# Performance work log

Hardware: AMD Instinct MI355X
Metric: run time of the kernel (lower is better)

The kernel has to match this reference:

```python
import jax, jax.numpy as jnp
import numpy as np

N = 50000      # nodes
E = 800000     # edges (avg degree 16)
D = 256        # d_model
H = 8          # heads
C = D // H     # per-head channels = 32
DE = 64        # edge feature dim
NEG_SLOPE = 0.2
EPS = 1e-5


def setup_inputs() -> dict:
    key = jax.random.key(0)
    ks = jax.random.split(key, 12)
    s = 0.05
    return {
        "x": jax.random.normal(ks[0], (N, D), jnp.float32),
        "edge_attr": jax.random.normal(ks[1], (E, DE), jnp.float32),
        "edge_index": jax.random.randint(ks[2], (2, E), 0, N, dtype=jnp.int32),
        # GATv2Conv params (torch Linear layout: [out, in])
        "W_l": jax.random.normal(ks[3], (H * C, D), jnp.float32) * s,   # lin_l (source)
        "b_l": jnp.zeros((H * C,), jnp.float32),
        "W_r": jax.random.normal(ks[4], (H * C, D), jnp.float32) * s,   # lin_r (target)
        "b_r": jnp.zeros((H * C,), jnp.float32),
        "W_e": jax.random.normal(ks[5], (H * C, DE), jnp.float32) * s,  # lin_edge (no bias)
        "att": jax.random.normal(ks[6], (H, C), jnp.float32) * s,       # attention vector a
        "W_res": jax.random.normal(ks[7], (H * C, D), jnp.float32) * s, # residual Linear (no bias)
        "bias": jnp.zeros((H * C,), jnp.float32),                        # conv output bias
        "gamma": jnp.ones((D,), jnp.float32),                            # LayerNorm weight
        "beta": jnp.zeros((D,), jnp.float32),                            # LayerNorm bias
    }


def reference(x, edge_attr, W_l, b_l, W_r, b_r, W_e, att, W_res, bias, gamma, beta, edge_index):
    src = edge_index[0]  # j (messages flow source -> target)
    dst = edge_index[1]  # i

    xl = (x @ W_l.T + b_l).reshape(N, H, C)   # source transform
    xr = (x @ W_r.T + b_r).reshape(N, H, C)   # target transform
    ee = (edge_attr @ W_e.T).reshape(E, H, C)  # edge embedding

    # GATv2 attention logits per edge/head
    g = jax.nn.leaky_relu(xl[src] + xr[dst] + ee, NEG_SLOPE)  # [E, H, C]
    alpha = jnp.einsum("ehc,hc->eh", g, att)                   # [E, H]

    # segment softmax over incoming edges of each target node
    amax = jax.ops.segment_max(alpha, dst, num_segments=N)     # [N, H] (-inf for empty)
    ealpha = jnp.exp(alpha - amax[dst])
    denom = jax.ops.segment_sum(ealpha, dst, num_segments=N)   # [N, H]
    alpha = ealpha / jnp.where(denom > 0, denom, 1.0)[dst]

    # weighted message aggregation (scatter-add)
    msg = xl[src] * alpha[:, :, None]                          # [E, H, C]
    out = jax.ops.segment_sum(msg, dst, num_segments=N)        # [N, H, C]

    out = out.reshape(N, H * C) + x @ W_res.T + bias           # concat heads + residual + bias

    # LayerNorm over last dim
    mu = out.mean(-1, keepdims=True)
    var = ((out - mu) ** 2).mean(-1, keepdims=True)
    return (out - mu) * jax.lax.rsqrt(var + EPS) * gamma + beta
```

## Files before the change

### kernel.cpp

```cpp
#include <hip/hip_runtime.h>

#define N_NODES 50000
#define N_EDGES 800000
#define D_MODEL 256
#define H_HEADS 8
#define C_CH 32
#define DE_DIM 64
#define NEG_SLOPE 0.2f
#define LN_EPS 1e-5f
#define TILES (N_EDGES / 64)
#define AGG_K 32

typedef float  f32x4  __attribute__((ext_vector_type(4)));
typedef short  bf16x8 __attribute__((ext_vector_type(8)));

static __device__ __forceinline__ unsigned short f2bf(float f) {
    unsigned int u = __float_as_uint(f);
    u += 0x7fffu + ((u >> 16) & 1u);
    return (unsigned short)(u >> 16);
}
static __device__ __forceinline__ float bf2f(unsigned short s) {
    return __uint_as_float(((unsigned int)s) << 16);
}
static __device__ __forceinline__ bf16x8 load_cvt8(const float* __restrict__ p) {
    float4 a = *(const float4*)p;
    float4 b = *(const float4*)(p + 4);
    bf16x8 r;
    r[0] = (short)f2bf(a.x); r[1] = (short)f2bf(a.y);
    r[2] = (short)f2bf(a.z); r[3] = (short)f2bf(a.w);
    r[4] = (short)f2bf(b.x); r[5] = (short)f2bf(b.y);
    r[6] = (short)f2bf(b.z); r[7] = (short)f2bf(b.w);
    return r;
}

__global__ __launch_bounds__(256) void cvt_bf16_kernel(const float* __restrict__ in,
                                                       unsigned short* __restrict__ out,
                                                       int n8) {
    int g = blockIdx.x * 256 + threadIdx.x;
    if (g < n8) {
        bf16x8 v = load_cvt8(in + (size_t)g * 8);
        *(bf16x8*)(out + (size_t)g * 8) = v;
    }
}

__global__ __launch_bounds__(256) void node_gemm(const unsigned short* __restrict__ xbf,
                                                 const unsigned short* __restrict__ Wbf,
                                                 const float* __restrict__ bl,
                                                 const float* __restrict__ br,
                                                 unsigned short* __restrict__ xl,
                                                 unsigned short* __restrict__ xr,
                                                 float* __restrict__ res) {
    int tid = threadIdx.x;
    int lane = tid & 63, wv = tid >> 6;
    int quad = lane >> 4, l15 = lane & 15;
    int rowTile = blockIdx.x * 64;
    int which = blockIdx.y;
    const unsigned short* W = Wbf + (size_t)which * 65536;
    int colBase = wv * 64;

    f32x4 acc[4][4];
#pragma unroll
    for (int r = 0; r < 4; r++)
#pragma unroll
        for (int c = 0; c < 4; c++) acc[r][c] = (f32x4){0.f, 0.f, 0.f, 0.f};

#pragma unroll 1
    for (int k8 = 0; k8 < 8; ++k8) {
        int kb = k8 * 32 + quad * 8;
        bf16x8 af[4], bfr[4];
#pragma unroll
        for (int r = 0; r < 4; r++) {
            int row = rowTile + r * 16 + l15;
            if (row > N_NODES - 1) row = N_NODES - 1;
            af[r] = *(const bf16x8*)(xbf + (size_t)row * D_MODEL + kb);
        }
#pragma unroll
        for (int c = 0; c < 4; c++) {
            int col = colBase + c * 16 + l15;
            bfr[c] = *(const bf16x8*)(W + (size_t)col * D_MODEL + kb);
        }
#pragma unroll
        for (int r = 0; r < 4; r++)
#pragma unroll
            for (int c = 0; c < 4; c++)
                acc[r][c] = __builtin_amdgcn_mfma_f32_16x16x32_bf16(af[r], bfr[c], acc[r][c], 0, 0, 0);
    }

    float bv[4];
#pragma unroll
    for (int c = 0; c < 4; c++) {
        int col = colBase + c * 16 + l15;
        bv[c] = (which == 0) ? bl[col] : (which == 1 ? br[col] : 0.f);
    }
#pragma unroll
    for (int r = 0; r < 4; r++) {
#pragma unroll
        for (int g = 0; g < 4; g++) {
            int row = rowTile + r * 16 + quad * 4 + g;
            if (row < N_NODES) {
#pragma unroll
                for (int c = 0; c < 4; c++) {
                    int col = colBase + c * 16 + l15;
                    float v = acc[r][c][g] + bv[c];
                    size_t idx = (size_t)row * D_MODEL + col;
                    if (which == 0)      xl[idx] = f2bf(v);
                    else if (which == 1) xr[idx] = f2bf(v);
                    else                 res[idx] = v;
                }
            }
        }
    }
}

__global__ __launch_bounds__(256) void edge_logits(const float* __restrict__ edge_attr,
                                                   const float* __restrict__ We,
                                                   const float* __restrict__ att,
                                                   const int* __restrict__ srcIdx,
                                                   const int* __restrict__ dstIdx,
                                                   const int* __restrict__ posOf,
                                                   const unsigned short* __restrict__ xl,
                                                   const unsigned short* __restrict__ xr,
                                                   float* __restrict__ alphaP) {
    __shared__ short weS[2048 * 8];
    __shared__ float attS[256];
    __shared__ short aS[4][128 * 8];

    int tid = threadIdx.x;
    int lane = tid & 63, wv = tid >> 6;
    int quad = lane >> 4, l15 = lane & 15;

    for (int g = tid; g < 2048; g += 256) {
        int c = g >> 7, kq = (g >> 6) & 1, ln = g & 63;
        int o = c * 16 + (ln & 15);
        int k = kq * 32 + (ln >> 4) * 8;
        bf16x8 v = load_cvt8(We + o * DE_DIM + k);
        *(bf16x8*)&weS[g * 8] = v;
    }
    if (tid < 256) attS[tid] = att[tid];
    __syncthreads();

    for (int tile = blockIdx.x; tile < TILES; tile += gridDim.x) {
        int e0 = tile * 64 + wv * 16;
#pragma unroll
        for (int kq = 0; kq < 2; ++kq) {
            int e = e0 + l15;
            int k = kq * 32 + quad * 8;
            bf16x8 v = load_cvt8(edge_attr + (size_t)e * DE_DIM + k);
            *(bf16x8*)&aS[wv][(kq * 64 + lane) * 8] = v;
        }
        int srcv[4], dstv[4], posv[4];
#pragma unroll
        for (int r = 0; r < 4; r++) {
            int e = e0 + quad * 4 + r;
            srcv[r] = srcIdx[e];
            dstv[r] = dstIdx[e];
            posv[r] = posOf[e];
        }
        __syncthreads();

        bf16x8 a0 = *(bf16x8*)&aS[wv][(0 * 64 + lane) * 8];
        bf16x8 a1 = *(bf16x8*)&aS[wv][(1 * 64 + lane) * 8];

        float pa[4][8];
#pragma unroll
        for (int r = 0; r < 4; r++)
#pragma unroll
            for (int h = 0; h < 8; h++) pa[r][h] = 0.f;

#pragma unroll
        for (int c = 0; c < 16; c++) {
            bf16x8 b0 = *(bf16x8*)&weS[((c * 2 + 0) * 64 + lane) * 8];
            bf16x8 b1 = *(bf16x8*)&weS[((c * 2 + 1) * 64 + lane) * 8];
            f32x4 ee = (f32x4){0.f, 0.f, 0.f, 0.f};
            ee = __builtin_amdgcn_mfma_f32_16x16x32_bf16(a0, b0, ee, 0, 0, 0);
            ee = __builtin_amdgcn_mfma_f32_16x16x32_bf16(a1, b1, ee, 0, 0, 0);
            int col = c * 16 + l15;
            float attv = attS[col];
#pragma unroll
            for (int r = 0; r < 4; r++) {
                float xlv = bf2f(xl[(size_t)srcv[r] * D_MODEL + col]);
                float xrv = bf2f(xr[(size_t)dstv[r] * D_MODEL + col]);
                float t = ee[r] + xlv + xrv;
                t = (t > 0.f) ? t : NEG_SLOPE * t;
                pa[r][c >> 1] += t * attv;
            }
        }
#pragma unroll
        for (int r = 0; r < 4; r++)
#pragma unroll
            for (int h = 0; h < 8; h++) {
                float v = pa[r][h];
                v += __shfl_xor(v, 1);
                v += __shfl_xor(v, 2);
                v += __shfl_xor(v, 4);
                v += __shfl_xor(v, 8);
                pa[r][h] = v;
            }
        if (l15 == 0) {
#pragma unroll
            for (int r = 0; r < 4; r++) {
#pragma unroll
                for (int h = 0; h < 8; h++)
                    alphaP[(size_t)posv[r] * 8 + h] = pa[r][h];
            }
        }
        __syncthreads();
    }
}

__global__ __launch_bounds__(256) void hist_kernel(const int* __restrict__ dstIdx,
                                                   int* __restrict__ cnt) {
    int e = blockIdx.x * 256 + threadIdx.x;
    if (e < N_EDGES) atomicAdd(&cnt[dstIdx[e]], 1);
}

__global__ __launch_bounds__(1024) void scan_kernel(const int* __restrict__ cnt,
                                                    int* __restrict__ off,
                                                    int* __restrict__ woff) {
    const int CHUNK = 49;
    int tid = threadIdx.x;
    int base = tid * CHUNK;
    int local[CHUNK];
    int sum = 0;
#pragma unroll
    for (int j = 0; j < CHUNK; ++j) {
        int idx = base + j;
        int v = (idx < N_NODES) ? cnt[idx] : 0;
        local[j] = sum;
        sum += v;
    }
    int lane = tid & 63, wv = tid >> 6;
    int s = sum;
#pragma unroll
    for (int ofs = 1; ofs < 64; ofs <<= 1) {
        int t2 = __shfl_up(s, ofs);
        if (lane >= ofs) s += t2;
    }
    __shared__ int wsum[16];
    __shared__ int woffS[16];
    if (lane == 63) wsum[wv] = s;
    __syncthreads();
    if (tid == 0) {
        int a = 0;
#pragma unroll
        for (int i = 0; i < 16; ++i) { woffS[i] = a; a += wsum[i]; }
    }
    __syncthreads();
    int excl = woffS[wv] + (s - sum);
#pragma unroll
    for (int j = 0; j < CHUNK; ++j) {
        int idx = base + j;
        if (idx < N_NODES) {
            int v = excl + local[j];
            off[idx] = v;
            woff[idx] = v;
        }
    }
    if (tid == 0) off[N_NODES] = N_EDGES;
}

__global__ __launch_bounds__(256) void scatter_kernel(const int* __restrict__ srcIdx,
                                                      const int* __restrict__ dstIdx,
                                                      int* __restrict__ woff,
                                                      int* __restrict__ posOf,
                                                      int* __restrict__ srcP) {
    int e = blockIdx.x * 256 + threadIdx.x;
    if (e < N_EDGES) {
        int pos = atomicAdd(&woff[dstIdx[e]], 1);
        posOf[e] = pos;
        srcP[pos] = srcIdx[e];
    }
}

__global__ __launch_bounds__(256) void aggregate_ln(const int* __restrict__ off,
                                                    const int* __restrict__ srcP,
                                                    const float* __restrict__ alphaP,
                                                    const unsigned short* __restrict__ xl,
                                                    const float* __restrict__ res,
                                                    const float* __restrict__ biasc,
                                                    const float* __restrict__ gamma,
                                                    const float* __restrict__ beta,
                                                    float* __restrict__ out) {
    int i = blockIdx.x;
    int t = threadIdx.x;
    int h = t >> 5;
    int beg = off[i], end = off[i + 1];

    __shared__ float wS[AGG_K * 8];
    __shared__ int srcS[AGG_K];

    float s = 0.f, acc = 0.f;
    for (int ch = beg; ch < end; ch += AGG_K) {
        int n = min(AGG_K, end - ch);
        __syncthreads();
        if (t < n * 8) wS[t] = __expf(alphaP[(size_t)ch * 8 + t]);
        if (t < n)     srcS[t] = srcP[ch + t];
        __syncthreads();
#pragma unroll 4
        for (int p = 0; p < n; ++p) {
            float w = wS[p * 8 + h];
            s += w;
            acc += w * bf2f(xl[(size_t)srcS[p] * D_MODEL + t]);
        }
    }
    float v = (end > beg) ? (acc / s) : 0.f;
    v += res[(size_t)i * D_MODEL + t] + biasc[t];

    __shared__ float rs[4], rq[4];
    float sum = v, sq = v * v;
#pragma unroll
    for (int msk = 32; msk >= 1; msk >>= 1) {
        sum += __shfl_xor(sum, msk);
        sq  += __shfl_xor(sq, msk);
    }
    int lane = t & 63, wv = t >> 6;
    __syncthreads();
    if (lane == 0) { rs[wv] = sum; rq[wv] = sq; }
    __syncthreads();
    float tot  = rs[0] + rs[1] + rs[2] + rs[3];
    float totq = rq[0] + rq[1] + rq[2] + rq[3];
    float mu  = tot * (1.f / 256.f);
    float var = totq * (1.f / 256.f) - mu * mu;
    var = fmaxf(var, 0.f);
    float inv = rsqrtf(var + LN_EPS);
    out[(size_t)i * D_MODEL + t] = (v - mu) * inv * gamma[t] + beta[t];
}

extern "C" void kernel_launch(void* const* d_in, const int* in_sizes, int n_in,
                              void* d_out, int out_size, void* d_ws, size_t ws_size,
                              hipStream_t stream) {
    const float* x         = (const float*)d_in[0];
    const float* edge_attr = (const float*)d_in[1];
    const int*   edge_index= (const int*)d_in[2];
    const float* Wl        = (const float*)d_in[3];
    const float* bl        = (const float*)d_in[4];
    const float* Wr        = (const float*)d_in[5];
    const float* br        = (const float*)d_in[6];
    const float* We        = (const float*)d_in[7];
    const float* att       = (const float*)d_in[8];
    const float* Wres      = (const float*)d_in[9];
    const float* biasc     = (const float*)d_in[10];
    const float* gamma     = (const float*)d_in[11];
    const float* beta      = (const float*)d_in[12];
    const int* srcIdx = edge_index;
    const int* dstIdx = edge_index + N_EDGES;
    float* out = (float*)d_out;

    char* ws = (char*)d_ws;
    unsigned short* xl  = (unsigned short*)ws;
    unsigned short* xr  = xl + (size_t)N_NODES * D_MODEL;
    unsigned short* xbf = xr + (size_t)N_NODES * D_MODEL;
    unsigned short* Wbf = xbf + (size_t)N_NODES * D_MODEL;
    float* res    = (float*)(Wbf + 3 * 65536);
    float* alphaP = res + (size_t)N_NODES * D_MODEL;
    int* cnt   = (int*)(alphaP + (size_t)N_EDGES * 8);
    int* off   = cnt + N_NODES;
    int* woff  = off + (N_NODES + 1);
    int* posOf = woff + N_NODES;
    int* srcP  = posOf + N_EDGES;
    (void)ws_size; (void)n_in; (void)in_sizes; (void)out_size;

    hipMemsetAsync(cnt, 0, N_NODES * sizeof(int), stream);

    cvt_bf16_kernel<<<(N_NODES * D_MODEL / 8 + 255) / 256, 256, 0, stream>>>(x, xbf, N_NODES * D_MODEL / 8);
    cvt_bf16_kernel<<<32, 256, 0, stream>>>(Wl,   Wbf,             65536 / 8);
    cvt_bf16_kernel<<<32, 256, 0, stream>>>(Wr,   Wbf + 65536,     65536 / 8);
    cvt_bf16_kernel<<<32, 256, 0, stream>>>(Wres, Wbf + 2 * 65536, 65536 / 8);

    dim3 g1((N_NODES + 63) / 64, 3);
    node_gemm<<<g1, 256, 0, stream>>>(xbf, Wbf, bl, br, xl, xr, res);

    hist_kernel<<<(N_EDGES + 255) / 256, 256, 0, stream>>>(dstIdx, cnt);
    scan_kernel<<<1, 1024, 0, stream>>>(cnt, off, woff);
    scatter_kernel<<<(N_EDGES + 255) / 256, 256, 0, stream>>>(srcIdx, dstIdx, woff, posOf, srcP);

    edge_logits<<<1280, 256, 0, stream>>>(edge_attr, We, att, srcIdx, dstIdx, posOf, xl, xr, alphaP);

    aggregate_ln<<<N_NODES, 256, 0, stream>>>(off, srcP, alphaP, xl, res,
                                              biasc, gamma, beta, out);
}
```

Measured before the change: 891.3 us.

## Transpose edge MFMA operands and use one wave per node in aggregation

The edge_logits kernel swaps the MFMA operand order so each lane owns a single edge and four contiguous channels. That turns the scattered bf16 gathers of xl/xr into vectorized ushort4 loads, and it removes the LDS staging of edge_attr, the per-tile __syncthreads and the wide shuffle reductions. The aggregate_ln kernel now assigns one wavefront per node with four channels per lane. It prefetches the next source index and logit in registers and reduces LayerNorm statistics with wave shuffles only, dropping LDS and block barriers. The trade-off is more redundant exp work per lane and a serial edge loop per wave, which loses some cross-edge parallelism for high-degree nodes.

```diff
diff --git a/kernel.cpp b/kernel.cpp
--- a/kernel.cpp
+++ b/kernel.cpp
@@ -9,7 +9,6 @@
 #define NEG_SLOPE 0.2f
 #define LN_EPS 1e-5f
 #define TILES (N_EDGES / 64)
-#define AGG_K 32
 
 typedef float  f32x4  __attribute__((ext_vector_type(4)));
 typedef short  bf16x8 __attribute__((ext_vector_type(8)));
@@ -122,8 +121,6 @@
                                                    const unsigned short* __restrict__ xr,
                                                    float* __restrict__ alphaP) {
     __shared__ short weS[2048 * 8];
-    __shared__ float attS[256];
-    __shared__ short aS[4][128 * 8];
 
     int tid = threadIdx.x;
     int lane = tid & 63, wv = tid >> 6;
@@ -136,75 +133,63 @@
         bf16x8 v = load_cvt8(We + o * DE_DIM + k);
         *(bf16x8*)&weS[g * 8] = v;
     }
-    if (tid < 256) attS[tid] = att[tid];
     __syncthreads();
 
     for (int tile = blockIdx.x; tile < TILES; tile += gridDim.x) {
-        int e0 = tile * 64 + wv * 16;
-#pragma unroll
-        for (int kq = 0; kq < 2; ++kq) {
-            int e = e0 + l15;
-            int k = kq * 32 + quad * 8;
-            bf16x8 v = load_cvt8(edge_attr + (size_t)e * DE_DIM + k);
-            *(bf16x8*)&aS[wv][(kq * 64 + lane) * 8] = v;
-        }
-        int srcv[4], dstv[4], posv[4];
-#pragma unroll
-        for (int r = 0; r < 4; r++) {
-            int e = e0 + quad * 4 + r;
-            srcv[r] = srcIdx[e];
-            dstv[r] = dstIdx[e];
-            posv[r] = posOf[e];
-        }
-        __syncthreads();
-
-        bf16x8 a0 = *(bf16x8*)&aS[wv][(0 * 64 + lane) * 8];
-        bf16x8 a1 = *(bf16x8*)&aS[wv][(1 * 64 + lane) * 8];
-
-        float pa[4][8];
-#pragma unroll
-        for (int r = 0; r < 4; r++)
-#pragma unroll
-            for (int h = 0; h < 8; h++) pa[r][h] = 0.f;
+        int e = tile * 64 + wv * 16 + l15;
+        int srcv = srcIdx[e];
+        int dstv = dstIdx[e];
+        int posv = posOf[e];
+
+        bf16x8 a0 = load_cvt8(edge_attr + (size_t)e * DE_DIM + quad * 8);
+        bf16x8 a1 = load_cvt8(edge_attr + (size_t)e * DE_DIM + 32 + quad * 8);
+
+        const unsigned short* xlr = xl + (size_t)srcv * D_MODEL + quad * 4;
+        const unsigned short* xrr = xr + (size_t)dstv * D_MODEL + quad * 4;
+
+        float pa[8];
+#pragma unroll
+        for (int h = 0; h < 8; h++) pa[h] = 0.f;
 
 #pragma unroll
         for (int c = 0; c < 16; c++) {
             bf16x8 b0 = *(bf16x8*)&weS[((c * 2 + 0) * 64 + lane) * 8];
             bf16x8 b1 = *(bf16x8*)&weS[((c * 2 + 1) * 64 + lane) * 8];
             f32x4 ee = (f32x4){0.f, 0.f, 0.f, 0.f};
-            ee = __builtin_amdgcn_mfma_f32_16x16x32_bf16(a0, b0, ee, 0, 0, 0);
-            ee = __builtin_amdgcn_mfma_f32_16x16x32_bf16(a1, b1, ee, 0, 0, 0);
-            int col = c * 16 + l15;
-            float attv = attS[col];
-#pragma unroll
-            for (int r = 0; r < 4; r++) {
-                float xlv = bf2f(xl[(size_t)srcv[r] * D_MODEL + col]);
-                float xrv = bf2f(xr[(size_t)dstv[r] * D_MODEL + col]);
-                float t = ee[r] + xlv + xrv;
-                t = (t > 0.f) ? t : NEG_SLOPE * t;
-                pa[r][c >> 1] += t * attv;
-            }
-        }
-#pragma unroll
-        for (int r = 0; r < 4; r++)
-#pragma unroll
-            for (int h = 0; h < 8; h++) {
-                float v = pa[r][h];
-                v += __shfl_xor(v, 1);
-                v += __shfl_xor(v, 2);
-                v += __shfl_xor(v, 4);
-                v += __shfl_xor(v, 8);
-                pa[r][h] = v;
-            }
-        if (l15 == 0) {
-#pragma unroll
-            for (int r = 0; r < 4; r++) {
-#pragma unroll
-                for (int h = 0; h < 8; h++)
-                    alphaP[(size_t)posv[r] * 8 + h] = pa[r][h];
-            }
-        }
-        __syncthreads();
+            ee = __builtin_amdgcn_mfma_f32_16x16x32_bf16(b0, a0, ee, 0, 0, 0);
+            ee = __builtin_amdgcn_mfma_f32_16x16x32_bf16(b1, a1, ee, 0, 0, 0);
+            ushort4 x4 = *(const ushort4*)(xlr + c * 16);
+            ushort4 r4 = *(const ushort4*)(xrr + c * 16);
+            f32x4 av = *(const f32x4*)(att + c * 16 + quad * 4);
+            float s = 0.f;
+            float t0 = ee[0] + bf2f(x4.x) + bf2f(r4.x);
+            float t1 = ee[1] + bf2f(x4.y) + bf2f(r4.y);
+            float t2 = ee[2] + bf2f(x4.z) + bf2f(r4.z);
+            float t3 = ee[3] + bf2f(x4.w) + bf2f(r4.w);
+            t0 = (t0 > 0.f) ? t0 : NEG_SLOPE * t0;
+            t1 = (t1 > 0.f) ? t1 : NEG_SLOPE * t1;
+            t2 = (t2 > 0.f) ? t2 : NEG_SLOPE * t2;
+            t3 = (t3 > 0.f) ? t3 : NEG_SLOPE * t3;
+            s = fmaf(t0, av[0], s);
+            s = fmaf(t1, av[1], s);
+            s = fmaf(t2, av[2], s);
+            s = fmaf(t3, av[3], s);
+            pa[c >> 1] += s;
+        }
+#pragma unroll
+        for (int h = 0; h < 8; h++) {
+            float v = pa[h];
+            v += __shfl_xor(v, 16);
+            v += __shfl_xor(v, 32);
+            pa[h] = v;
+        }
+        if (quad == 0) {
+            float4 w0 = make_float4(pa[0], pa[1], pa[2], pa[3]);
+            *(float4*)(alphaP + (size_t)posv * 8) = w0;
+        } else if (quad == 1) {
+            float4 w1 = make_float4(pa[4], pa[5], pa[6], pa[7]);
+            *(float4*)(alphaP + (size_t)posv * 8 + 4) = w1;
+        }
     }
 }
 
@@ -281,49 +266,64 @@
                                                     const float* __restrict__ gamma,
                                                     const float* __restrict__ beta,
                                                     float* __restrict__ out) {
-    int i = blockIdx.x;
-    int t = threadIdx.x;
-    int h = t >> 5;
+    int wv = threadIdx.x >> 6, lane = threadIdx.x & 63;
+    int i = blockIdx.x * 4 + wv;
     int beg = off[i], end = off[i + 1];
-
-    __shared__ float wS[AGG_K * 8];
-    __shared__ int srcS[AGG_K];
-
-    float s = 0.f, acc = 0.f;
-    for (int ch = beg; ch < end; ch += AGG_K) {
-        int n = min(AGG_K, end - ch);
-        __syncthreads();
-        if (t < n * 8) wS[t] = __expf(alphaP[(size_t)ch * 8 + t]);
-        if (t < n)     srcS[t] = srcP[ch + t];
-        __syncthreads();
-#pragma unroll 4
-        for (int p = 0; p < n; ++p) {
-            float w = wS[p * 8 + h];
-            s += w;
-            acc += w * bf2f(xl[(size_t)srcS[p] * D_MODEL + t]);
-        }
-    }
-    float v = (end > beg) ? (acc / s) : 0.f;
-    v += res[(size_t)i * D_MODEL + t] + biasc[t];
-
-    __shared__ float rs[4], rq[4];
-    float sum = v, sq = v * v;
+    int h = lane >> 3;
+
+    float acc0 = 0.f, acc1 = 0.f, acc2 = 0.f, acc3 = 0.f, s = 0.f;
+
+    int p = beg;
+    int src_n = 0; float a_n = 0.f;
+    if (p < end) {
+        src_n = srcP[p];
+        a_n   = alphaP[(size_t)p * 8 + h];
+    }
+    while (p < end) {
+        int src = src_n; float a = a_n;
+        int pn = p + 1;
+        if (pn < end) {
+            src_n = srcP[pn];
+            a_n   = alphaP[(size_t)pn * 8 + h];
+        }
+        ushort4 v = *(const ushort4*)(xl + (size_t)src * D_MODEL + lane * 4);
+        float w = __expf(a);
+        s += w;
+        acc0 = fmaf(w, bf2f(v.x), acc0);
+        acc1 = fmaf(w, bf2f(v.y), acc1);
+        acc2 = fmaf(w, bf2f(v.z), acc2);
+        acc3 = fmaf(w, bf2f(v.w), acc3);
+        p = pn;
+    }
+
+    float rs = (end > beg) ? (1.f / s) : 0.f;
+    float4 r4 = *(const float4*)(res + (size_t)i * D_MODEL + lane * 4);
+    float4 b4 = *(const float4*)(biasc + lane * 4);
+    float v0 = acc0 * rs + r4.x + b4.x;
+    float v1 = acc1 * rs + r4.y + b4.y;
+    float v2 = acc2 * rs + r4.z + b4.z;
+    float v3 = acc3 * rs + r4.w + b4.w;
+
+    float sum = v0 + v1 + v2 + v3;
+    float sq  = v0 * v0 + v1 * v1 + v2 * v2 + v3 * v3;
 #pragma unroll
     for (int msk = 32; msk >= 1; msk >>= 1) {
         sum += __shfl_xor(sum, msk);
         sq  += __shfl_xor(sq, msk);
     }
-    int lane = t & 63, wv = t >> 6;
-    __syncthreads();
-    if (lane == 0) { rs[wv] = sum; rq[wv] = sq; }
-    __syncthreads();
-    float tot  = rs[0] + rs[1] + rs[2] + rs[3];
-    float totq = rq[0] + rq[1] + rq[2] + rq[3];
-    float mu  = tot * (1.f / 256.f);
-    float var = totq * (1.f / 256.f) - mu * mu;
+    float mu  = sum * (1.f / 256.f);
+    float var = sq * (1.f / 256.f) - mu * mu;
     var = fmaxf(var, 0.f);
     float inv = rsqrtf(var + LN_EPS);
-    out[(size_t)i * D_MODEL + t] = (v - mu) * inv * gamma[t] + beta[t];
+
+    float4 g4 = *(const float4*)(gamma + lane * 4);
+    float4 be4 = *(const float4*)(beta + lane * 4);
+    float4 o4;
+    o4.x = (v0 - mu) * inv * g4.x + be4.x;
+    o4.y = (v1 - mu) * inv * g4.y + be4.y;
+    o4.z = (v2 - mu) * inv * g4.z + be4.z;
+    o4.w = (v3 - mu) * inv * g4.w + be4.w;
+    *(float4*)(out + (size_t)i * D_MODEL + lane * 4) = o4;
 }
 
 extern "C" void kernel_launch(void* const* d_in, const int* in_sizes, int n_in,
@@ -376,6 +376,6 @@
 
     edge_logits<<<1280, 256, 0, stream>>>(edge_attr, We, att, srcIdx, dstIdx, posOf, xl, xr, alphaP);
 
-    aggregate_ln<<<N_NODES, 256, 0, stream>>>(off, srcP, alphaP, xl, res,
-                                              biasc, gamma, beta, out);
-}
+    aggregate_ln<<<N_NODES / 4, 256, 0, stream>>>(off, srcP, alphaP, xl, res,
+                                                  biasc, gamma, beta, out);
+}
```

Result: slower. 974.5 us (+9.3%).
